# Kernel optimization log

Hardware: AMD Instinct MI355X
Metric: run time of the kernel (lower is better)

Reference implementation:

```python
import jax, jax.numpy as jnp
import numpy as np

EPS = 1e-5

def layernorm(x, g, b):
    mu = jnp.mean(x, axis=-1, keepdims=True)
    var = jnp.var(x, axis=-1, keepdims=True)
    return (x - mu) * jax.lax.rsqrt(var + EPS) * g + b

def setup_inputs() -> dict:
    B, S, H = 8, 2048, 1024
    key = jax.random.key(0)
    ks = jax.random.split(key, 8)
    lim = 1.0 / np.sqrt(2 * H)  # torch Linear default init scale
    return {
        "input_states": jax.random.normal(ks[0], (B, S, H), jnp.float32),
        "in_g": jnp.ones((H,), jnp.float32), "in_b": jnp.zeros((H,), jnp.float32),
        "st_g": jnp.ones((H,), jnp.float32), "st_b": jnp.zeros((H,), jnp.float32),
        "Wu": jax.random.uniform(ks[1], (H, 2 * H), jnp.float32, -lim, lim),
        "bu": jax.random.uniform(ks[2], (H,), jnp.float32, -lim, lim),
        "Wr": jax.random.uniform(ks[3], (H, 2 * H), jnp.float32, -lim, lim),
        "br": jax.random.uniform(ks[4], (H,), jnp.float32, -lim, lim),
        "Wo": jax.random.uniform(ks[5], (H, 2 * H), jnp.float32, -lim, lim),
        "bo": jax.random.uniform(ks[6], (H,), jnp.float32, -lim, lim),
        "ln_g": jnp.ones((H,), jnp.float32), "ln_b": jnp.zeros((H,), jnp.float32),
    }

def reference(input_states, in_g, in_b, st_g, st_b, Wu, bu, Wr, br, Wo, bo, ln_g, ln_b):
    B, S, H = input_states.shape
    xn = layernorm(input_states, in_g, in_b)            # [B,S,H]
    h0 = jnp.zeros((B, H), input_states.dtype)
    nh0 = layernorm(h0, st_g, st_b)                     # = st_b (zeros input)

    def step(carry, x_t):
        h, nh = carry
        comb = jnp.concatenate([x_t, nh], axis=-1)      # [B,2H]
        u = jax.nn.sigmoid(comb @ Wu.T + bu)
        r = jax.nn.sigmoid(comb @ Wr.T + br)
        comb2 = jnp.concatenate([x_t, r * nh], axis=-1)
        c = jnp.tanh(comb2 @ Wo.T + bo)
        h = (1.0 - u) * h + u * c
        nh = layernorm(h, st_g, st_b)
        return (h, nh), h                               # dropout is identity (eval)

    _, hs = jax.lax.scan(step, (h0, nh0), jnp.swapaxes(xn, 0, 1))  # hs: [S,B,H]
    outputs = jnp.swapaxes(hs, 0, 1)                    # [B,S,H]
    return layernorm(outputs, ln_g, ln_b)
```

## Files before the change

kernel.cpp:

```cpp
#include <hip/hip_runtime.h>


typedef unsigned short bf16_t;
typedef unsigned int u32_t;
typedef u32_t u32x2 __attribute__((ext_vector_type(2)));
typedef u32_t u32x4 __attribute__((ext_vector_type(4)));

__device__ __forceinline__ float bf2f(bf16_t u) {
    return __uint_as_float(((unsigned)u) << 16);
}
__device__ __forceinline__ float bf2f_hi(u32_t d) {
    return __uint_as_float(d & 0xFFFF0000u);
}
__device__ __forceinline__ float bf2f_lo(u32_t d) {
    return __uint_as_float(d << 16);
}
__device__ __forceinline__ bf16_t f2bf(float f) {
    unsigned u = __float_as_uint(f);
    unsigned r = (u + 0x7FFFu + ((u >> 16) & 1u)) >> 16;
    return (bf16_t)r;
}

#define B_  8
#define S_  2048
#define H_  1024
#define EPS 1e-5f
#define NB  256
#define NT  512
#define SENT 0xFFFFu
#define GUARD_MAX 1500000L

template<bool SC1>
__device__ __forceinline__ void tstore(u32_t* p, u32_t v) {
    if (SC1) asm volatile("global_store_dword %0, %1, off sc0 sc1" :: "v"(p), "v"(v) : "memory");
    else     asm volatile("global_store_dword %0, %1, off sc0"     :: "v"(p), "v"(v) : "memory");
}
template<bool SC1>
__device__ __forceinline__ void tload2(u32x2& v, const u32_t* p) {
    if (SC1) asm volatile("global_load_dwordx2 %0, %1, off sc0 sc1" : "=v"(v) : "v"(p));
    else     asm volatile("global_load_dwordx2 %0, %1, off sc0"     : "=v"(v) : "v"(p));
}
template<bool SC1>
__device__ __forceinline__ void tload4(u32x4& v, const u32_t* p) {
    if (SC1) asm volatile("global_load_dwordx4 %0, %1, off sc0 sc1" : "=v"(v) : "v"(p));
    else     asm volatile("global_load_dwordx4 %0, %1, off sc0"     : "=v"(v) : "v"(p));
}
template<bool SC1>
__device__ __forceinline__ u32x2 poll2(const u32_t* p, u32_t tag, long& guard) {
    u32x2 v;
    if (guard > GUARD_MAX) {
        tload2<SC1>(v, p);
        asm volatile("s_waitcnt vmcnt(0)" ::: "memory");
        return v;
    }
    for (;;) {
        tload2<SC1>(v, p);
        asm volatile("s_waitcnt vmcnt(0)" ::: "memory");
        __builtin_amdgcn_sched_barrier(0);
        if ((((v.x ^ tag) | (v.y ^ tag)) & 0xFFFFu) == 0) break;
        __builtin_amdgcn_s_sleep(1);
        if (++guard > GUARD_MAX) break;
    }
    return v;
}

__device__ __forceinline__ float dot8(u32x4 W, float4 n0, float4 n1) {
    return bf2f_lo(W.x) * n0.x + bf2f_hi(W.x) * n0.y
         + bf2f_lo(W.y) * n0.z + bf2f_hi(W.y) * n0.w
         + bf2f_lo(W.z) * n1.x + bf2f_hi(W.z) * n1.y
         + bf2f_lo(W.w) * n1.z + bf2f_hi(W.w) * n1.w;
}

__device__ __forceinline__ int rdv(u32_t* cnt, unsigned need, int tid, int* sdead) {
    __syncthreads();
    if (tid == 0) {
        __hip_atomic_fetch_add(cnt, 1u, __ATOMIC_ACQ_REL, __HIP_MEMORY_SCOPE_AGENT);
        long g = 0;
        while (__hip_atomic_load(cnt, __ATOMIC_ACQUIRE, __HIP_MEMORY_SCOPE_AGENT) < need) {
            __builtin_amdgcn_s_sleep(2);
            if (++g > 3000000L) { *sdead = 1; break; }
        }
    }
    __syncthreads();
    return *sdead;
}

__global__ void detect_flag(const unsigned* __restrict__ in_g_bits, int* flag,
                            u32_t* __restrict__ epoch) {
    *flag = (in_g_bits[0] == 0x3F800000u) ? 0 : 1;
    *epoch = *epoch + 1u;
}

__global__ __launch_bounds__(256) void canon_vec(
    const void* v0, const void* v1, const void* v2, const void* v3,
    const void* v4, const void* v5, const void* v6, const void* v7,
    const void* v8, float* __restrict__ dst, const int* __restrict__ flagp)
{
    int isbf = *flagp;
    const void* srcs[9] = {v0, v1, v2, v3, v4, v5, v6, v7, v8};
    const void* s = srcs[blockIdx.y];
    int k = blockIdx.x * 256 + threadIdx.x;
    float val = isbf ? bf2f(((const bf16_t*)s)[k]) : ((const float*)s)[k];
    dst[(long)blockIdx.y * H_ + k] = val;
}

__global__ __launch_bounds__(256) void canon_wh(
    const void* Wu, const void* Wr, const void* Wo,
    bf16_t* __restrict__ Whu, bf16_t* __restrict__ Whr, bf16_t* __restrict__ Who,
    const int* __restrict__ flagp)
{
    int isbf = *flagp;
    const void* srcs[3] = {Wu, Wr, Wo};
    bf16_t* dsts[3] = {Whu, Whr, Who};
    const void* s = srcs[blockIdx.y];
    bf16_t* d = dsts[blockIdx.y];
    long j = blockIdx.x;
#pragma unroll
    for (int i = 0; i < 4; i++) {
        int k = threadIdx.x + i * 256;
        long off = j * (2 * H_) + H_ + k;
        bf16_t v = isbf ? ((const bf16_t*)s)[off] : f2bf(((const float*)s)[off]);
        d[j * H_ + k] = v;
    }
}

__global__ __launch_bounds__(256) void ln_in(
    const void* __restrict__ src, const float* __restrict__ g,
    const float* __restrict__ bt, bf16_t* __restrict__ dst,
    const int* __restrict__ flagp)
{
    int isbf = *flagp;
    long row = blockIdx.x;
    float v[4];
    float s = 0.f, q = 0.f;
#pragma unroll
    for (int i = 0; i < 4; i++) {
        long idx = row * H_ + threadIdx.x + i * 256;
        v[i] = isbf ? bf2f(((const bf16_t*)src)[idx]) : ((const float*)src)[idx];
        s += v[i];
        q += v[i] * v[i];
    }
#pragma unroll
    for (int off = 32; off; off >>= 1) {
        s += __shfl_down(s, off);
        q += __shfl_down(q, off);
    }
    __shared__ float ls[4], lq[4];
    __shared__ float smu, sri;
    int wid = threadIdx.x >> 6, lane = threadIdx.x & 63;
    if (lane == 0) { ls[wid] = s; lq[wid] = q; }
    __syncthreads();
    if (threadIdx.x == 0) {
        float S = ls[0] + ls[1] + ls[2] + ls[3];
        float Q = lq[0] + lq[1] + lq[2] + lq[3];
        float mu = S * (1.f / H_);
        smu = mu;
        sri = rsqrtf(Q * (1.f / H_) - mu * mu + EPS);
    }
    __syncthreads();
    float mu = smu, ri = sri;
#pragma unroll
    for (int i = 0; i < 4; i++) {
        int k = threadIdx.x + i * 256;
        dst[row * H_ + k] = f2bf((v[i] - mu) * ri * g[k] + bt[k]);
    }
}

__global__ __launch_bounds__(256) void ln_out(
    void* __restrict__ buf, const float* __restrict__ g,
    const float* __restrict__ bt, const int* __restrict__ flagp)
{
    int isbf = *flagp;
    long row = blockIdx.x;
    float v[4];
    float s = 0.f, q = 0.f;
#pragma unroll
    for (int i = 0; i < 4; i++) {
        long idx = row * H_ + threadIdx.x + i * 256;
        v[i] = isbf ? bf2f(((const bf16_t*)buf)[idx]) : ((const float*)buf)[idx];
        s += v[i];
        q += v[i] * v[i];
    }
#pragma unroll
    for (int off = 32; off; off >>= 1) {
        s += __shfl_down(s, off);
        q += __shfl_down(q, off);
    }
    __shared__ float ls[4], lq[4];
    __shared__ float smu, sri;
    int wid = threadIdx.x >> 6, lane = threadIdx.x & 63;
    if (lane == 0) { ls[wid] = s; lq[wid] = q; }
    __syncthreads();
    if (threadIdx.x == 0) {
        float S = ls[0] + ls[1] + ls[2] + ls[3];
        float Q = lq[0] + lq[1] + lq[2] + lq[3];
        float mu = S * (1.f / H_);
        smu = mu;
        sri = rsqrtf(Q * (1.f / H_) - mu * mu + EPS);
    }
    __syncthreads();
    float mu = smu, ri = sri;
#pragma unroll
    for (int i = 0; i < 4; i++) {
        long idx = row * H_ + threadIdx.x + i * 256;
        int k = threadIdx.x + i * 256;
        float o = (v[i] - mu) * ri * g[k] + bt[k];
        if (isbf) ((bf16_t*)buf)[idx] = f2bf(o);
        else      ((float*)buf)[idx] = o;
    }
}

__global__ __launch_bounds__(256) void gemm_pre(
    const bf16_t* __restrict__ A,
    const void* __restrict__ Wu, const void* __restrict__ Wr, const void* __restrict__ Wo,
    const float* __restrict__ bias3,
    bf16_t* __restrict__ Pu, bf16_t* __restrict__ Pr, bf16_t* __restrict__ Po,
    const int* __restrict__ flagp)
{
    int isbf = *flagp;
    const void* W;
    const float* bias = bias3 + (long)blockIdx.z * H_;
    bf16_t* C;
    if (blockIdx.z == 0)      { W = Wu; C = Pu; }
    else if (blockIdx.z == 1) { W = Wr; C = Pr; }
    else                      { W = Wo; C = Po; }

    __shared__ float sa[8][128];
    __shared__ float sb[8][128];
    float acc[8][8];
#pragma unroll
    for (int i = 0; i < 8; i++)
#pragma unroll
        for (int j = 0; j < 8; j++) acc[i][j] = 0.f;

    int tx = threadIdx.x % 16, ty = threadIdx.x / 16;
    int m0 = blockIdx.x * 128, n0 = blockIdx.y * 128;
    int lr = threadIdx.x >> 1;
    int lc = (threadIdx.x & 1) * 4;

    for (int kt = 0; kt < H_; kt += 8) {
        ushort4 av = *(const ushort4*)(A + (long)(m0 + lr) * H_ + kt + lc);
        float w0, w1, w2, w3;
        long woff = (long)(n0 + lr) * (2 * H_) + kt + lc;
        if (isbf) {
            ushort4 bv = *(const ushort4*)((const bf16_t*)W + woff);
            w0 = bf2f(bv.x); w1 = bf2f(bv.y); w2 = bf2f(bv.z); w3 = bf2f(bv.w);
        } else {
            float4 bv = *(const float4*)((const float*)W + woff);
            w0 = bv.x; w1 = bv.y; w2 = bv.z; w3 = bv.w;
        }
        sa[lc + 0][lr] = bf2f(av.x); sa[lc + 1][lr] = bf2f(av.y);
        sa[lc + 2][lr] = bf2f(av.z); sa[lc + 3][lr] = bf2f(av.w);
        sb[lc + 0][lr] = w0; sb[lc + 1][lr] = w1;
        sb[lc + 2][lr] = w2; sb[lc + 3][lr] = w3;
        __syncthreads();
#pragma unroll
        for (int k = 0; k < 8; k++) {
            float ar[8], brg[8];
#pragma unroll
            for (int i = 0; i < 8; i++) ar[i] = sa[k][ty * 8 + i];
#pragma unroll
            for (int j = 0; j < 8; j++) brg[j] = sb[k][tx * 8 + j];
#pragma unroll
            for (int i = 0; i < 8; i++)
#pragma unroll
                for (int j = 0; j < 8; j++) acc[i][j] += ar[i] * brg[j];
        }
        __syncthreads();
    }
#pragma unroll
    for (int i = 0; i < 8; i++) {
        long m = m0 + ty * 8 + i;
#pragma unroll
        for (int j = 0; j < 8; j++) {
            int n = n0 + tx * 8 + j;
            C[m * H_ + n] = f2bf(acc[i][j] + bias[n]);
        }
    }
}

template<bool SC1>
__device__ __forceinline__ void scan_loop(
    int b, int j0, int tid, int isbf,
    const bf16_t* __restrict__ Whu, const bf16_t* __restrict__ Whr,
    const bf16_t* __restrict__ Who,
    const bf16_t* __restrict__ Pu, const bf16_t* __restrict__ Pr,
    const bf16_t* __restrict__ Po,
    u32_t* __restrict__ h_tagb, u32_t* __restrict__ rnh_tagb,
    void* __restrict__ outv,
    const float* __restrict__ g_s, const float* __restrict__ bta_s,
    float* __restrict__ nh_s, float* __restrict__ u_s,
    float* __restrict__ ls, float* __restrict__ lq)
{
    const int w = tid >> 6, l = tid & 63;

    const int dotA  = w * 8 + (l >> 3);
    const int pA    = l & 7;
    const int gate  = dotA >> 5;
    const int colLA = dotA & 31;
    const int colA  = j0 + colLA;
    const bf16_t* WA = gate ? Whr : Whu;
    const bf16_t* PA = gate ? Pr : Pu;
    u32x4 wa[16];
    {
        const u32x4* src = (const u32x4*)(WA + (long)colA * H_ + pA * 128);
#pragma unroll
        for (int i = 0; i < 16; i++) wa[i] = src[i];
    }
    const int colLB = w * 4 + (l >> 4);
    const int colB  = j0 + colLB;
    const int oB    = l & 15;
    u32x4 wb[8];
    {
        const u32x4* src = (const u32x4*)(Who + (long)colB * H_ + oB * 64);
#pragma unroll
        for (int i = 0; i < 8; i++) wb[i] = src[i];
    }

    float* nh_row = nh_s + w * 132;
    const bool ldrA = (pA == 0);
    const bool ldrB = (oB == 0);
    u32_t* h_my  = h_tagb + colB;
    u32_t* rn_my = rnh_tagb + colA;
    const u32_t* h_pollp  = h_tagb + tid * 2;
    const u32_t* rn_pollp = rnh_tagb + tid * 2;

    float h_reg = 0.f;
    long guard = 0;

    for (int t = 0; t < S_; t++) {
        float pvalA = 0.f, povalB = 0.f;
        if (ldrA) pvalA = bf2f(PA[((long)b * S_ + t) * H_ + colA]);
        if (ldrB) povalB = bf2f(Po[((long)b * S_ + t) * H_ + colB]);

        if (t == 0) {
            *(float2*)(nh_row + 2 * l) = *(const float2*)(bta_s + tid * 2);
        } else {
            u32x2 hv = poll2<SC1>(h_pollp, (u32_t)t, guard);
            float x0 = bf2f_hi(hv.x), x1 = bf2f_hi(hv.y);
            float s = x0 + x1, q = x0 * x0 + x1 * x1;
#pragma unroll
            for (int off = 32; off; off >>= 1) {
                s += __shfl_xor(s, off);
                q += __shfl_xor(q, off);
            }
            if (l == 0) { ls[w] = s; lq[w] = q; }
            __syncthreads();
            float S = 0.f, Q = 0.f;
#pragma unroll
            for (int i = 0; i < 8; i++) { S += ls[i]; Q += lq[i]; }
            float mu = S * (1.f / H_);
            float ri = rsqrtf(Q * (1.f / H_) - mu * mu + EPS);
            int k = tid * 2;
            float2 gg = *(const float2*)(g_s + k);
            float2 bb = *(const float2*)(bta_s + k);
            float2 o;
            o.x = (x0 - mu) * ri * gg.x + bb.x;
            o.y = (x1 - mu) * ri * gg.y + bb.y;
            *(float2*)(nh_row + 2 * l) = o;
        }
        __syncthreads();

        float accA = 0.f;
        {
            const float* nb = nh_s + pA * 132;
#pragma unroll
            for (int i = 0; i < 16; i++) {
                float4 n0 = ((const float4*)(nb + i * 8))[0];
                float4 n1 = ((const float4*)(nb + i * 8))[1];
                accA += dot8(wa[i], n0, n1);
            }
        }
#pragma unroll
        for (int off = 1; off <= 4; off <<= 1) accA += __shfl_xor(accA, off);
        if (ldrA) {
            float sg = 1.f / (1.f + __expf(-(pvalA + accA)));
            if (gate == 0) {
                u_s[colLA] = sg;
            } else {
                float rv = sg * nh_s[(colA >> 7) * 132 + (colA & 127)];
                tstore<SC1>(rn_my, ((u32_t)f2bf(rv) << 16) | (u32_t)(t + 1));
            }
        }
        __syncthreads();

        {
            u32x2 rv2 = poll2<SC1>(rn_pollp, (u32_t)(t + 1), guard);
            float2 o;
            o.x = bf2f_hi(rv2.x);
            o.y = bf2f_hi(rv2.y);
            *(float2*)(nh_row + 2 * l) = o;
        }
        __syncthreads();

        float accB = 0.f;
        {
            const float* nb = nh_s + (oB >> 1) * 132 + (oB & 1) * 64;
#pragma unroll
            for (int i = 0; i < 8; i++) {
                float4 n0 = ((const float4*)(nb + i * 8))[0];
                float4 n1 = ((const float4*)(nb + i * 8))[1];
                accB += dot8(wb[i], n0, n1);
            }
        }
#pragma unroll
        for (int off = 1; off <= 8; off <<= 1) accB += __shfl_xor(accB, off);
        if (ldrB) {
            float c = tanhf(povalB + accB);
            float u = u_s[colLB];
            h_reg = h_reg + u * (c - h_reg);
            tstore<SC1>(h_my, ((u32_t)f2bf(h_reg) << 16) | (u32_t)(t + 1));
            long op = ((long)b * S_ + t) * H_ + colB;
            if (isbf) ((bf16_t*)outv)[op] = f2bf(h_reg);
            else      ((float*)outv)[op]  = h_reg;
        }
        __syncthreads();
    }
}

__global__ __launch_bounds__(NT, 2) void scan_persist(
    const bf16_t* __restrict__ Whu, const bf16_t* __restrict__ Whr,
    const bf16_t* __restrict__ Who,
    const float* __restrict__ st_g, const float* __restrict__ st_b,
    const bf16_t* __restrict__ Pu, const bf16_t* __restrict__ Pr,
    const bf16_t* __restrict__ Po,
    u32_t* __restrict__ h_tag, u32_t* __restrict__ rnh_tag,
    void* __restrict__ outv, const int* __restrict__ flagp,
    const u32_t* __restrict__ epochp,
    u32_t* __restrict__ probe, u32_t* __restrict__ xccpub,
    u32_t* __restrict__ cnt1, u32_t* __restrict__ cnt2,
    u32_t* __restrict__ slowf)
{
    __shared__ float g_s[H_], bta_s[H_];
    __shared__ float nh_s[8 * 132];
    __shared__ float u_s[32];
    __shared__ float ls[8], lq[8];
    __shared__ int s_dead, s_g1, s_tok, s_bad, s_fast, s_xcc;

    const int tid = threadIdx.x;
    const int blk = blockIdx.x;
    const int isbf = *flagp;
    const u32_t ep = *epochp;

    const int b    = blk & 7;
    const int slot = blk >> 3;
    const int j0   = slot * 32;
    u32_t* h_tagb   = h_tag   + (long)b * H_;
    u32_t* rnh_tagb = rnh_tag + (long)b * H_;

    __threadfence();

    for (int i = tid; i < H_; i += NT) { g_s[i] = st_g[i]; bta_s[i] = st_b[i]; }
    if (tid == 0) {
        s_dead = 0; s_g1 = 1; s_tok = 0; s_bad = 0; s_fast = 0;
        int x;
        asm volatile("s_getreg_b32 %0, hwreg(HW_REG_XCC_ID)" : "=s"(x));
        s_xcc = x & 0xF;
    }
    __syncthreads();

    if (tid < 32) {
        tstore<true>(h_tagb   + j0 + tid, SENT);
        tstore<true>(rnh_tagb + j0 + tid, SENT);
    }
    if (tid == 0) tstore<true>(xccpub + ((long)b * 32 + slot) * 16, (u32_t)s_xcc);
    asm volatile("s_waitcnt vmcnt(0)" ::: "memory");

    if (rdv(cnt1 + b, 32u, tid, &s_dead)) return;

    if (tid < 64) {
        u32_t v;
        const u32_t* pp = xccpub + ((long)b * 32 + (tid & 31)) * 16;
        asm volatile("global_load_dword %0, %1, off sc0 sc1" : "=v"(v) : "v"(pp));
        asm volatile("s_waitcnt vmcnt(0)" ::: "memory");
        __builtin_amdgcn_sched_barrier(0);
        bool ok = (tid >= 32) || (v == (u32_t)s_xcc);
        if (__ballot(ok) != ~0ull && tid == 0) s_g1 = 0;
    }
    __syncthreads();

    if (s_g1) {
        if (tid == 0) {
            tstore<false>(probe + ((long)b * 32 + slot) * 16, ep);
            asm volatile("s_waitcnt vmcnt(0)" ::: "memory");
        }
        __syncthreads();
        if (tid < 64) {
            const u32_t* pp = probe + ((long)b * 32 + (tid & 31)) * 16;
            bool ok = false;
            long it = 0;
            for (;;) {
                u32_t v;
                asm volatile("global_load_dword %0, %1, off sc0" : "=v"(v) : "v"(pp));
                asm volatile("s_waitcnt vmcnt(0)" ::: "memory");
                __builtin_amdgcn_sched_barrier(0);
                ok = (tid >= 32) || (v == ep);
                if (__ballot(ok) == ~0ull) break;
                __builtin_amdgcn_s_sleep(2);
                if (++it > 20000L) break;
            }
            if (tid == 0) s_tok = (__ballot(ok) == ~0ull) ? 1 : 0;
        }
    }
    __syncthreads();

    if (s_g1 && s_tok) {
        const u32_t* sp = (tid < 256) ? (h_tagb + tid * 4)
                                      : (rnh_tagb + (tid - 256) * 4);
        u32x4 a;
        tload4<false>(a, sp);
        asm volatile("s_waitcnt vmcnt(0)" ::: "memory");
        __builtin_amdgcn_sched_barrier(0);
        if (a.x != SENT || a.y != SENT || a.z != SENT || a.w != SENT)
            s_bad = 1;
    }
    __syncthreads();

    if (tid == 0) {
        int fastwant = s_g1 && s_tok && !s_bad;
        if (!fastwant)
            __hip_atomic_fetch_add(slowf + b, 1u, __ATOMIC_ACQ_REL,
                                   __HIP_MEMORY_SCOPE_AGENT);
    }
    if (rdv(cnt2 + b, 32u, tid, &s_dead)) return;
    if (tid == 0)
        s_fast = (__hip_atomic_load(slowf + b, __ATOMIC_ACQUIRE,
                                    __HIP_MEMORY_SCOPE_AGENT) == 0u) ? 1 : 0;
    __syncthreads();

    if (s_fast)
        scan_loop<false>(b, j0, tid, isbf, Whu, Whr, Who, Pu, Pr, Po,
                         h_tagb, rnh_tagb, outv, g_s, bta_s, nh_s, u_s, ls, lq);
    else
        scan_loop<true>(b, j0, tid, isbf, Whu, Whr, Who, Pu, Pr, Po,
                        h_tagb, rnh_tagb, outv, g_s, bta_s, nh_s, u_s, ls, lq);
}

extern "C" void kernel_launch(void* const* d_in, const int* in_sizes, int n_in,
                              void* d_out, int out_size, void* d_ws, size_t ws_size,
                              hipStream_t stream)
{
    const void* input = d_in[0];
    const void* in_g  = d_in[1];
    const void* in_b  = d_in[2];
    const void* st_g  = d_in[3];
    const void* st_b  = d_in[4];
    const void* Wu    = d_in[5];
    const void* bu    = d_in[6];
    const void* Wr    = d_in[7];
    const void* br    = d_in[8];
    const void* Wo    = d_in[9];
    const void* bo    = d_in[10];
    const void* ln_g  = d_in[11];
    const void* ln_b  = d_in[12];

    const long NTOK = (long)B_ * S_ * H_;

    char* base = (char*)d_ws;
    int*    flag    = (int*)base;
    u32_t*  epoch   = (u32_t*)(base + 64);
    u32_t*  cnt1    = (u32_t*)(base + 512);
    u32_t*  cnt2    = (u32_t*)(base + 640);
    u32_t*  slowf   = (u32_t*)(base + 768);
    u32_t*  h_tag   = (u32_t*)(base + 4096);
    u32_t*  rnh_tag = h_tag + (long)B_ * H_;
    float*  vecs    = (float*)(rnh_tag + (long)B_ * H_);
    float* c_stg   = vecs + 0 * H_;
    float* c_stb   = vecs + 1 * H_;
    float* c_ing   = vecs + 2 * H_;
    float* c_inb   = vecs + 3 * H_;
    float* c_lng   = vecs + 4 * H_;
    float* c_lnb   = vecs + 5 * H_;
    float* c_bias3 = vecs + 6 * H_;
    bf16_t* Whu = (bf16_t*)(vecs + 9 * H_);
    bf16_t* Whr = Whu + (long)H_ * H_;
    bf16_t* Who = Whr + (long)H_ * H_;
    bf16_t* Pu  = Who + (long)H_ * H_;
    bf16_t* Pr  = Pu + NTOK;
    bf16_t* Po  = Pr + NTOK;
    u32_t*  probe  = (u32_t*)(Po + NTOK);
    u32_t*  xccpub = probe + 8 * 32 * 16;

    bf16_t* xn = (bf16_t*)d_out;

    detect_flag<<<1, 1, 0, stream>>>((const unsigned*)in_g, flag, epoch);

    canon_vec<<<dim3(H_ / 256, 9), 256, 0, stream>>>(
        st_g, st_b, in_g, in_b, ln_g, ln_b, bu, br, bo, vecs, flag);
    canon_wh<<<dim3(H_, 3), 256, 0, stream>>>(Wu, Wr, Wo, Whu, Whr, Who, flag);

    hipMemsetAsync(base + 128, 0, 4096 - 128, stream);

    ln_in<<<B_ * S_, 256, 0, stream>>>(input, c_ing, c_inb, xn, flag);

    gemm_pre<<<dim3(128, 8, 3), 256, 0, stream>>>(
        xn, Wu, Wr, Wo, c_bias3, Pu, Pr, Po, flag);

    scan_persist<<<NB, NT, 0, stream>>>(
        Whu, Whr, Who, c_stg, c_stb, Pu, Pr, Po,
        h_tag, rnh_tag, d_out, flag, epoch, probe, xccpub, cnt1, cnt2, slowf);

    ln_out<<<B_ * S_, 256, 0, stream>>>(d_out, c_lng, c_lnb, flag);
}
```

Measured before the change: 13.39 ms.

## Assign scan batches dynamically by XCC via atomic slot claiming

The persistent scan kernel now launches twice as many blocks. Each block reads its XCC id and atomically claims one of 32 slots for the batch matching that XCC, so all 32 blocks of a batch sit on the same XCC. Blocks that find no free slot sleep, then try other batches, and exit if none remain. This replaces the static blockIdx-to-batch mapping and its same-XCC check, aiming for the fast non-coherent path more often, at the cost of launch overhead and the risk of deadlock or starvation if placement is uneven.

After: 12.29 ms. 1.09x faster.

```diff
diff --git a/kernel.cpp b/kernel.cpp
--- a/kernel.cpp
+++ b/kernel.cpp
@@ -25,10 +25,10 @@
 #define S_  2048
 #define H_  1024
 #define EPS 1e-5f
-#define NB  256
+#define NB  512
 #define NT  512
 #define SENT 0xFFFFu
-#define GUARD_MAX 1500000L
+#define GUARD_MAX 3000000L
 
 template<bool SC1>
 __device__ __forceinline__ void tstore(u32_t* p, u32_t v) {
@@ -78,7 +78,7 @@
         long g = 0;
         while (__hip_atomic_load(cnt, __ATOMIC_ACQUIRE, __HIP_MEMORY_SCOPE_AGENT) < need) {
             __builtin_amdgcn_s_sleep(2);
-            if (++g > 3000000L) { *sdead = 1; break; }
+            if (++g > 5000000L) { *sdead = 1; break; }
         }
     }
     __syncthreads();
@@ -427,7 +427,7 @@
     u32_t* __restrict__ h_tag, u32_t* __restrict__ rnh_tag,
     void* __restrict__ outv, const int* __restrict__ flagp,
     const u32_t* __restrict__ epochp,
-    u32_t* __restrict__ probe, u32_t* __restrict__ xccpub,
+    u32_t* __restrict__ probe, u32_t* __restrict__ slots,
     u32_t* __restrict__ cnt1, u32_t* __restrict__ cnt2,
     u32_t* __restrict__ slowf)
 {
@@ -435,51 +435,52 @@
     __shared__ float nh_s[8 * 132];
     __shared__ float u_s[32];
     __shared__ float ls[8], lq[8];
-    __shared__ int s_dead, s_g1, s_tok, s_bad, s_fast, s_xcc;
+    __shared__ int s_dead, s_tok, s_bad, s_fast, s_batch, s_slot;
 
     const int tid = threadIdx.x;
-    const int blk = blockIdx.x;
     const int isbf = *flagp;
     const u32_t ep = *epochp;
 
-    const int b    = blk & 7;
-    const int slot = blk >> 3;
-    const int j0   = slot * 32;
+    __threadfence();
+
+    if (tid == 0) {
+        s_dead = 0; s_tok = 0; s_bad = 0; s_fast = 0;
+        int x;
+        asm volatile("s_getreg_b32 %0, hwreg(HW_REG_XCC_ID)" : "=s"(x));
+        x &= 7;
+        int batch = -1, slot = 0;
+        unsigned s = atomicAdd(&slots[x], 1u);
+        if (s < 32u) { batch = x; slot = (int)s; }
+        else {
+            for (int wt = 0; wt < 40; wt++) __builtin_amdgcn_s_sleep(127);
+            for (int k = 1; k <= 8 && batch < 0; k++) {
+                int b2 = (x + k) & 7;
+                if (__hip_atomic_load(&slots[b2], __ATOMIC_RELAXED,
+                                      __HIP_MEMORY_SCOPE_AGENT) < 32u) {
+                    unsigned s2 = atomicAdd(&slots[b2], 1u);
+                    if (s2 < 32u) { batch = b2; slot = (int)s2; }
+                }
+            }
+        }
+        s_batch = batch; s_slot = slot;
+    }
+    __syncthreads();
+    if (s_batch < 0) return;
+    const int b = s_batch, j0 = s_slot * 32, slot = s_slot;
     u32_t* h_tagb   = h_tag   + (long)b * H_;
     u32_t* rnh_tagb = rnh_tag + (long)b * H_;
 
-    __threadfence();
-
     for (int i = tid; i < H_; i += NT) { g_s[i] = st_g[i]; bta_s[i] = st_b[i]; }
-    if (tid == 0) {
-        s_dead = 0; s_g1 = 1; s_tok = 0; s_bad = 0; s_fast = 0;
-        int x;
-        asm volatile("s_getreg_b32 %0, hwreg(HW_REG_XCC_ID)" : "=s"(x));
-        s_xcc = x & 0xF;
-    }
-    __syncthreads();
 
     if (tid < 32) {
         tstore<true>(h_tagb   + j0 + tid, SENT);
         tstore<true>(rnh_tagb + j0 + tid, SENT);
     }
-    if (tid == 0) tstore<true>(xccpub + ((long)b * 32 + slot) * 16, (u32_t)s_xcc);
     asm volatile("s_waitcnt vmcnt(0)" ::: "memory");
 
     if (rdv(cnt1 + b, 32u, tid, &s_dead)) return;
 
-    if (tid < 64) {
-        u32_t v;
-        const u32_t* pp = xccpub + ((long)b * 32 + (tid & 31)) * 16;
-        asm volatile("global_load_dword %0, %1, off sc0 sc1" : "=v"(v) : "v"(pp));
-        asm volatile("s_waitcnt vmcnt(0)" ::: "memory");
-        __builtin_amdgcn_sched_barrier(0);
-        bool ok = (tid >= 32) || (v == (u32_t)s_xcc);
-        if (__ballot(ok) != ~0ull && tid == 0) s_g1 = 0;
-    }
-    __syncthreads();
-
-    if (s_g1) {
+    {
         if (tid == 0) {
             tstore<false>(probe + ((long)b * 32 + slot) * 16, ep);
             asm volatile("s_waitcnt vmcnt(0)" ::: "memory");
@@ -504,7 +505,7 @@
     }
     __syncthreads();
 
-    if (s_g1 && s_tok) {
+    if (s_tok) {
         const u32_t* sp = (tid < 256) ? (h_tagb + tid * 4)
                                       : (rnh_tagb + (tid - 256) * 4);
         u32x4 a;
@@ -517,7 +518,7 @@
     __syncthreads();
 
     if (tid == 0) {
-        int fastwant = s_g1 && s_tok && !s_bad;
+        int fastwant = s_tok && !s_bad;
         if (!fastwant)
             __hip_atomic_fetch_add(slowf + b, 1u, __ATOMIC_ACQ_REL,
                                    __HIP_MEMORY_SCOPE_AGENT);
@@ -562,6 +563,7 @@
     u32_t*  cnt1    = (u32_t*)(base + 512);
     u32_t*  cnt2    = (u32_t*)(base + 640);
     u32_t*  slowf   = (u32_t*)(base + 768);
+    u32_t*  slots   = (u32_t*)(base + 896);
     u32_t*  h_tag   = (u32_t*)(base + 4096);
     u32_t*  rnh_tag = h_tag + (long)B_ * H_;
     float*  vecs    = (float*)(rnh_tag + (long)B_ * H_);
@@ -579,7 +581,6 @@
     bf16_t* Pr  = Pu + NTOK;
     bf16_t* Po  = Pr + NTOK;
     u32_t*  probe  = (u32_t*)(Po + NTOK);
-    u32_t*  xccpub = probe + 8 * 32 * 16;
 
     bf16_t* xn = (bf16_t*)d_out;
 
@@ -598,7 +599,7 @@
 
     scan_persist<<<NB, NT, 0, stream>>>(
         Whu, Whr, Who, c_stg, c_stb, Pu, Pr, Po,
-        h_tag, rnh_tag, d_out, flag, epoch, probe, xccpub, cnt1, cnt2, slowf);
+        h_tag, rnh_tag, d_out, flag, epoch, probe, slots, cnt1, cnt2, slowf);
 
     ln_out<<<B_ * S_, 256, 0, stream>>>(d_out, c_lng, c_lnb, flag);
 }
```
